# Kernel tuning notes

Hardware: AMD Instinct MI355X
Metric: run time of the kernel (lower is better)

The kernel has to match this reference:

```python
import jax, jax.numpy as jnp
import numpy as np

NUM_CODES = 8192
CODE_DIM = 64
DECAY = 0.99
EPSILON = 1e-05
COMMITMENT_COST = 0.25


def setup_inputs() -> dict:
    key = jax.random.key(0)
    k1, k2, k3 = jax.random.split(key, 3)
    z = jax.random.normal(k1, (32768, CODE_DIM), dtype=jnp.float32)
    emb = jax.random.normal(k2, (NUM_CODES, CODE_DIM), dtype=jnp.float32)
    emb = emb / jnp.linalg.norm(emb, axis=1, keepdims=True)
    return {
        "z": z,
        "embedding": emb,
        "ema_cluster_size": jnp.zeros((NUM_CODES,), dtype=jnp.float32),
        "ema_embedding": emb.copy(),
    }


def reference(z, embedding, ema_cluster_size, ema_embedding):
    z_flat = z.reshape(-1, CODE_DIM)  # [N, D]
    # squared euclidean distances [N, K]
    distances = (
        jnp.sum(z_flat * z_flat, axis=1, keepdims=True)
        - 2.0 * (z_flat @ embedding.T)
        + jnp.sum(embedding * embedding, axis=1)
    )
    indices = jnp.argmin(distances, axis=1)  # [N] int
    z_q = embedding[indices]  # [N, D] gather

    # EMA buffer updates (training path), expressed as pure outputs.
    counts = jax.ops.segment_sum(
        jnp.ones_like(indices, dtype=z_flat.dtype), indices, num_segments=NUM_CODES
    )  # encodings.sum(0)
    dw = jax.ops.segment_sum(z_flat, indices, num_segments=NUM_CODES)  # encodings.T @ z_flat
    new_cluster_size = DECAY * ema_cluster_size + (1.0 - DECAY) * counts
    new_ema_embedding = DECAY * ema_embedding + (1.0 - DECAY) * dw
    n = jnp.sum(new_cluster_size)
    cluster_size = (new_cluster_size + EPSILON) / (n + NUM_CODES * EPSILON) * n
    new_embedding = new_ema_embedding / cluster_size[:, None]

    z_q_full = z_q.reshape(z.shape)
    z_q_st = z + jax.lax.stop_gradient(z_q_full - z)  # straight-through
    vq_loss = COMMITMENT_COST * jnp.mean(
        (jax.lax.stop_gradient(z_q_full) - z) ** 2
    )
    return (z_q_st, indices, vq_loss, new_embedding, new_cluster_size, new_ema_embedding)
```

## Files before the change

### kernel.cpp

```cpp
#include <hip/hip_runtime.h>

typedef _Float16 half8 __attribute__((ext_vector_type(8)));
typedef float f32x4 __attribute__((ext_vector_type(4)));

#define N_PTS   32768
#define DIMS    64
#define K_CODES 8192

#define OUT_ZQ      0
#define OUT_IDX     2097152
#define OUT_LOSS    2129920
#define OUT_NEWEMB  2129921
#define OUT_NCS     2654209
#define OUT_NEWEMA  2662401

#define SC_EHI      0
#define SC_ELO      262144
#define SC_ENSC     524288
#define SC_VAL1     532480
#define SC_IDX1     794624
#define SC_VAL2     1056768
#define SC_FIXLIST  1318912
#define SC_SORTED   1323008
#define SC_OFFSETS  1355776

#define WS_COUNTS   0
#define WS_CURSOR   8192
#define WS_LOSS     16384
#define WS_NSUM     16385
#define WS_FIXCNT   16386
#define WS_ZERO_BYTES (16388u * 4u)
#define WS_NCS      16388
#define WS_ENORM    24580
#define WS_IDX      32772
#define WS_DW       65540

#define MARGIN_SCALED 16.0f

__device__ inline void gld16(const void* g, void* l) {
    __builtin_amdgcn_global_load_lds((const __attribute__((address_space(1))) unsigned*)g,
                                     (__attribute__((address_space(3))) unsigned*)l, 16, 0, 0);
}
__device__ inline void gld4(const void* g, void* l) {
    __builtin_amdgcn_global_load_lds((const __attribute__((address_space(1))) unsigned*)g,
                                     (__attribute__((address_space(3))) unsigned*)l, 4, 0, 0);
}

__global__ __launch_bounds__(256) void esplit_kernel(const float* __restrict__ emb,
                                                     float4* __restrict__ ehi4,
                                                     float4* __restrict__ elo4,
                                                     float* __restrict__ ensc,
                                                     float* __restrict__ enorm) {
    int k = blockIdx.x * 256 + threadIdx.x;
    const float4* e4 = reinterpret_cast<const float4*>(emb + (size_t)k * DIMS);
    float vals[64];
    float sum = 0.0f;
#pragma unroll
    for (int i = 0; i < 16; ++i) {
        float4 v = e4[i];
        vals[i*4+0] = v.x; vals[i*4+1] = v.y; vals[i*4+2] = v.z; vals[i*4+3] = v.w;
        sum = fmaf(v.x, v.x, sum); sum = fmaf(v.y, v.y, sum);
        sum = fmaf(v.z, v.z, sum); sum = fmaf(v.w, v.w, sum);
    }
    enorm[k] = sum;
    ensc[k]  = 65536.0f * sum;
#pragma unroll
    for (int c = 0; c < 8; ++c) {
        union { _Float16 h[8]; float4 v; } uh, ul;
#pragma unroll
        for (int j = 0; j < 8; ++j) {
            float X = 256.0f * vals[c*8+j];
            _Float16 hh = (_Float16)X;
            uh.h[j] = hh;
            ul.h[j] = (_Float16)(X - (float)hh);
        }
        int cc = c ^ (k & 7);
        ehi4[(size_t)k*8 + cc] = uh.v;
        elo4[(size_t)k*8 + cc] = ul.v;
    }
}

__global__ __launch_bounds__(256) void argmin_mfma(const float* __restrict__ z,
                                                   const char* __restrict__ ehi_g,
                                                   const char* __restrict__ elo_g,
                                                   const float* __restrict__ ensc_g,
                                                   float* __restrict__ val1,
                                                   int* __restrict__ idx1,
                                                   float* __restrict__ val2) {
    __shared__ __align__(16) char ebuf[2][2][8192];
    __shared__ float enb[2][64];

    const int tid = threadIdx.x;
    const int w   = tid >> 6;
    const int l   = tid & 63;
    const int l15 = l & 15;
    const int l4  = l >> 4;
    const int bid = blockIdx.x;
    const int rowbase = (bid >> 2) * 128 + w * 32;
    const int c0      = (bid & 3) * 2048;

    half8 ahi[2][2], alo[2][2];
#pragma unroll
    for (int s = 0; s < 2; ++s) {
        const float* zp = z + (size_t)(rowbase + s*16 + l15) * DIMS + l4 * 8;
#pragma unroll
        for (int ks = 0; ks < 2; ++ks) {
            float4 z0 = *reinterpret_cast<const float4*>(zp + ks*32);
            float4 z1 = *reinterpret_cast<const float4*>(zp + ks*32 + 4);
            float xv[8] = {z0.x, z0.y, z0.z, z0.w, z1.x, z1.y, z1.z, z1.w};
            half8 h, lo;
#pragma unroll
            for (int j = 0; j < 8; ++j) {
                float X = -512.0f * xv[j];
                _Float16 hh = (_Float16)X;
                h[j]  = hh;
                lo[j] = (_Float16)(X - (float)hh);
            }
            ahi[s][ks] = h; alo[s][ks] = lo;
        }
    }

    float b1[8], b2[8]; int i1[8];
#pragma unroll
    for (int r = 0; r < 8; ++r) { b1[r] = 3.4e38f; b2[r] = 3.4e38f; i1[r] = 0; }

    int rdoff[2];
#pragma unroll
    for (int ks = 0; ks < 2; ++ks)
        rdoff[ks] = l15 * 128 + (((ks*4 + l4) ^ (l15 & 7)) * 16);

    {
        const size_t gb = (size_t)c0 * 128;
        const char* sh = ehi_g + gb + tid*16;
        const char* sl = elo_g + gb + tid*16;
        char* dh = &ebuf[0][0][0] + w*1024;
        char* dl = &ebuf[0][1][0] + w*1024;
        gld16(sh,        dh);        gld16(sh + 4096, dh + 4096);
        gld16(sl,        dl);        gld16(sl + 4096, dl + 4096);
        if (w == 0) gld4(ensc_g + c0 + l, &enb[0][0]);
    }
    __syncthreads();

    int b = 0;
    for (int ch = 0; ch < 32; ++ch) {
        if (ch < 31) {
            const size_t gb = (size_t)(c0 + (ch+1)*64) * 128;
            const char* sh = ehi_g + gb + tid*16;
            const char* sl = elo_g + gb + tid*16;
            char* dh = &ebuf[b^1][0][0] + w*1024;
            char* dl = &ebuf[b^1][1][0] + w*1024;
            gld16(sh,        dh);        gld16(sh + 4096, dh + 4096);
            gld16(sl,        dl);        gld16(sl + 4096, dl + 4096);
            if (w == 0) gld4(ensc_g + c0 + (ch+1)*64 + l, &enb[b^1][0]);
        }
        const char* bhbase = &ebuf[b][0][0];
        const char* blbase = &ebuf[b][1][0];
#pragma unroll
        for (int t = 0; t < 4; ++t) {
            float en = enb[b][t*16 + l15];
            f32x4 envec = (f32x4){en, en, en, en};
            half8 bh[2], bl[2];
#pragma unroll
            for (int ks = 0; ks < 2; ++ks) {
                bh[ks] = *reinterpret_cast<const half8*>(bhbase + t*2048 + rdoff[ks]);
                bl[ks] = *reinterpret_cast<const half8*>(blbase + t*2048 + rdoff[ks]);
            }
            f32x4 acc[2];
            __builtin_amdgcn_s_setprio(1);
#pragma unroll
            for (int s = 0; s < 2; ++s)
                acc[s] = __builtin_amdgcn_mfma_f32_16x16x32_f16(ahi[s][0], bh[0], envec, 0, 0, 0);
#pragma unroll
            for (int s = 0; s < 2; ++s)
                acc[s] = __builtin_amdgcn_mfma_f32_16x16x32_f16(ahi[s][0], bl[0], acc[s], 0, 0, 0);
#pragma unroll
            for (int s = 0; s < 2; ++s)
                acc[s] = __builtin_amdgcn_mfma_f32_16x16x32_f16(alo[s][0], bh[0], acc[s], 0, 0, 0);
#pragma unroll
            for (int s = 0; s < 2; ++s)
                acc[s] = __builtin_amdgcn_mfma_f32_16x16x32_f16(ahi[s][1], bh[1], acc[s], 0, 0, 0);
#pragma unroll
            for (int s = 0; s < 2; ++s)
                acc[s] = __builtin_amdgcn_mfma_f32_16x16x32_f16(ahi[s][1], bl[1], acc[s], 0, 0, 0);
#pragma unroll
            for (int s = 0; s < 2; ++s)
                acc[s] = __builtin_amdgcn_mfma_f32_16x16x32_f16(alo[s][1], bh[1], acc[s], 0, 0, 0);
            __builtin_amdgcn_s_setprio(0);

            const int code = c0 + ch*64 + t*16 + l15;
#pragma unroll
            for (int s = 0; s < 2; ++s) {
#pragma unroll
                for (int j = 0; j < 4; ++j) {
                    const int r = s*4 + j;
                    float v = acc[s][j];
                    float nb2;
                    asm("v_med3_f32 %0, %1, %2, %3"
                        : "=v"(nb2) : "v"(b1[r]), "v"(b2[r]), "v"(v));
                    b2[r] = nb2;
                    bool c = v < b1[r];
                    b1[r] = c ? v : b1[r];
                    i1[r] = c ? code : i1[r];
                }
            }
        }
        __syncthreads();
        b ^= 1;
    }

#pragma unroll
    for (int m = 1; m < 16; m <<= 1) {
#pragma unroll
        for (int r = 0; r < 8; ++r) {
            float ob1 = __shfl_xor(b1[r], m, 64);
            int   oi1 = __shfl_xor(i1[r], m, 64);
            float ob2 = __shfl_xor(b2[r], m, 64);
            float nb2 = fminf(fminf(b2[r], ob2), fmaxf(b1[r], ob1));
            bool take = (ob1 < b1[r]) || (ob1 == b1[r] && oi1 < i1[r]);
            b1[r] = take ? ob1 : b1[r];
            i1[r] = take ? oi1 : i1[r];
            b2[r] = nb2;
        }
    }
    if (l15 == 0) {
        const int cs = bid & 3;
#pragma unroll
        for (int s = 0; s < 2; ++s)
#pragma unroll
            for (int j = 0; j < 4; ++j) {
                int row = rowbase + s*16 + l4*4 + j;
                int o = cs * N_PTS + row;
                val1[o] = b1[s*4+j];
                idx1[o] = i1[s*4+j];
                val2[o] = b2[s*4+j];
            }
    }
}

__global__ __launch_bounds__(256) void combine_kernel(const float* __restrict__ val1,
                                                      const int* __restrict__ idx1,
                                                      const float* __restrict__ val2,
                                                      int* __restrict__ ws_idx,
                                                      float* __restrict__ out_idxf,
                                                      int* __restrict__ fixcnt,
                                                      int* __restrict__ fixlist,
                                                      float* __restrict__ counts) {
    int row = blockIdx.x * 256 + threadIdx.x;
    float b1 = val1[row]; int i1 = idx1[row]; float b2 = val2[row];
#pragma unroll
    for (int c = 1; c < 4; ++c) {
        float ob1 = val1[c*N_PTS + row];
        int   oi1 = idx1[c*N_PTS + row];
        float ob2 = val2[c*N_PTS + row];
        float nb2 = fminf(fminf(b2, ob2), fmaxf(b1, ob1));
        if (ob1 < b1) { b1 = ob1; i1 = oi1; }
        b2 = nb2;
    }
    ws_idx[row]   = i1;
    out_idxf[row] = (float)i1;
    atomicAdd(&counts[i1], 1.0f);
    if (b2 - b1 < MARGIN_SCALED) {
        int p = atomicAdd(fixcnt, 1);
        if (p < 4096) fixlist[p] = row;
    }
}

__global__ __launch_bounds__(256) void fixup_kernel(const float* __restrict__ z,
                                                    const float* __restrict__ emb,
                                                    const float* __restrict__ enorm,
                                                    const int* __restrict__ fixcnt,
                                                    const int* __restrict__ fixlist,
                                                    int* __restrict__ ws_idx,
                                                    float* __restrict__ out_idxf,
                                                    float* __restrict__ counts) {
    __shared__ float zrow[64];
    __shared__ float rv[256];
    __shared__ int   ri[256];
    int cnt = *fixcnt; if (cnt > 4096) cnt = 4096;
    for (int g = blockIdx.x; g < cnt; g += 64) {
        int row = fixlist[g];
        __syncthreads();
        if (threadIdx.x < 64) zrow[threadIdx.x] = z[(size_t)row * DIMS + threadIdx.x];
        __syncthreads();
        float best = 3.4e38f; int bi = 0;
        for (int k = threadIdx.x; k < K_CODES; k += 256) {
            const float4* e4 = reinterpret_cast<const float4*>(emb + (size_t)k * DIMS);
            float s = 0.0f;
#pragma unroll
            for (int i = 0; i < 16; ++i) {
                float4 ev = e4[i];
                s = fmaf(zrow[i*4+0], ev.x, s);
                s = fmaf(zrow[i*4+1], ev.y, s);
                s = fmaf(zrow[i*4+2], ev.z, s);
                s = fmaf(zrow[i*4+3], ev.w, s);
            }
            float d = fmaf(-2.0f, s, enorm[k]);
            if (d < best) { best = d; bi = k; }
        }
        rv[threadIdx.x] = best; ri[threadIdx.x] = bi;
        __syncthreads();
        for (int off = 128; off > 0; off >>= 1) {
            if (threadIdx.x < off) {
                float ov = rv[threadIdx.x + off]; int oi = ri[threadIdx.x + off];
                if (ov < rv[threadIdx.x] || (ov == rv[threadIdx.x] && oi < ri[threadIdx.x])) {
                    rv[threadIdx.x] = ov; ri[threadIdx.x] = oi;
                }
            }
            __syncthreads();
        }
        if (threadIdx.x == 0) {
            int old = ws_idx[row];
            if (ri[0] != old) {
                atomicAdd(&counts[old], -1.0f);
                atomicAdd(&counts[ri[0]], 1.0f);
                ws_idx[row] = ri[0];
                out_idxf[row] = (float)ri[0];
            }
        }
    }
}

__global__ __launch_bounds__(256) void scan_cs_kernel(const float* __restrict__ ema_cs,
                                                      const float* __restrict__ counts,
                                                      float* __restrict__ ncs_ws,
                                                      float* __restrict__ out_ncs,
                                                      float* __restrict__ nsum,
                                                      int* __restrict__ offsets) {
    __shared__ int excl[256];
    __shared__ int tot[256];
    __shared__ float fpart[256];
    const int t = threadIdx.x;
    const int base = t * 32;
    int loc[32];
    int run = 0;
    float fs = 0.0f;
#pragma unroll
    for (int i = 0; i < 32; ++i) {
        float c = counts[base + i];
        float v = fmaf(0.99f, ema_cs[base + i], 0.01f * c);
        ncs_ws[base + i] = v;
        out_ncs[base + i] = v;
        fs += v;
        loc[i] = run;
        run += (int)c;
    }
    tot[t] = run;
    fpart[t] = fs;
    __syncthreads();
    if (t == 0) {
        int r = 0;
        float f = 0.0f;
        for (int i = 0; i < 256; ++i) { excl[i] = r; r += tot[i]; f += fpart[i]; }
        nsum[0] = f;
    }
    __syncthreads();
    const int off = excl[t];
#pragma unroll
    for (int i = 0; i < 32; ++i) offsets[base + i] = off + loc[i];
}

__global__ __launch_bounds__(256) void place_kernel(const int* __restrict__ idx,
                                                    const int* __restrict__ offsets,
                                                    int* __restrict__ cursor,
                                                    int* __restrict__ sorted) {
    int p = blockIdx.x * 256 + threadIdx.x;
    int k = idx[p];
    int pos = offsets[k] + atomicAdd(&cursor[k], 1);
    sorted[pos] = p;
}

__global__ __launch_bounds__(256) void dw_kernel(const float* __restrict__ z,
                                                 const int* __restrict__ sorted,
                                                 const int* __restrict__ offsets,
                                                 const float* __restrict__ counts,
                                                 float* __restrict__ dw) {
    const int w = threadIdx.x >> 6;
    const int lane = threadIdx.x & 63;
    const int k = blockIdx.x * 4 + w;
    const int start = offsets[k];
    const int cnt = (int)counts[k];
    float s = 0.0f;
    for (int i = 0; i < cnt; ++i) {
        int p = sorted[start + i];
        s += z[(size_t)p * DIMS + lane];
    }
    dw[(size_t)k * DIMS + lane] = s;
}

__global__ __launch_bounds__(256) void scatter_light(const float* __restrict__ z,
                                                     const float* __restrict__ emb,
                                                     const int* __restrict__ idx,
                                                     float* __restrict__ zq_out,
                                                     float* __restrict__ loss_accum) {
    const int tid = threadIdx.x;
    const int p = blockIdx.x * 64 + (tid >> 2);
    const int q = tid & 3;
    const int k = idx[p];

    const float4* zp = reinterpret_cast<const float4*>(z + (size_t)p * DIMS + q * 16);
    const float4* ep = reinterpret_cast<const float4*>(emb + (size_t)k * DIMS + q * 16);
    float4* op = reinterpret_cast<float4*>(zq_out + (size_t)p * DIMS + q * 16);

    float lsum = 0.0f;
#pragma unroll
    for (int i = 0; i < 4; ++i) {
        float4 zv = zp[i];
        float4 ev = ep[i];
        float4 t;
        t.x = ev.x - zv.x; t.y = ev.y - zv.y; t.z = ev.z - zv.z; t.w = ev.w - zv.w;
        lsum = fmaf(t.x, t.x, lsum); lsum = fmaf(t.y, t.y, lsum);
        lsum = fmaf(t.z, t.z, lsum); lsum = fmaf(t.w, t.w, lsum);
        float4 o;
        o.x = zv.x + t.x; o.y = zv.y + t.y; o.z = zv.z + t.z; o.w = zv.w + t.w;
        op[i] = o;
    }
#pragma unroll
    for (int o = 32; o > 0; o >>= 1) lsum += __shfl_down(lsum, o);
    if ((tid & 63) == 0) atomicAdd(loss_accum, lsum);
}

__global__ __launch_bounds__(256) void final_kernel(const float* __restrict__ ema_emb,
                                                    const float* __restrict__ dw,
                                                    const float* __restrict__ ncs,
                                                    const float* __restrict__ n_ptr,
                                                    const float* __restrict__ loss_ptr,
                                                    float* __restrict__ out_newemb,
                                                    float* __restrict__ out_newema,
                                                    float* __restrict__ out_loss) {
    const int i = blockIdx.x * 256 + threadIdx.x;
    const int k = i >> 6;
    const float n = *n_ptr;
    const float cs = (ncs[k] + 1e-5f) / (n + (float)K_CODES * 1e-5f) * n;
    const float ne = fmaf(0.99f, ema_emb[i], 0.01f * dw[i]);
    out_newema[i] = ne;
    out_newemb[i] = ne / cs;
    if (i == 0) out_loss[0] = 0.25f * (loss_ptr[0] / 2097152.0f);
}

extern "C" void kernel_launch(void* const* d_in, const int* in_sizes, int n_in,
                              void* d_out, int out_size, void* d_ws, size_t ws_size,
                              hipStream_t stream) {
    const float* z       = (const float*)d_in[0];
    const float* emb     = (const float*)d_in[1];
    const float* ema_cs  = (const float*)d_in[2];
    const float* ema_emb = (const float*)d_in[3];
    float* out = (float*)d_out;
    float* ws  = (float*)d_ws;

    float* counts  = ws + WS_COUNTS;
    int*   cursor  = (int*)(ws + WS_CURSOR);
    float* loss    = ws + WS_LOSS;
    float* nsum    = ws + WS_NSUM;
    int*   fixcnt  = (int*)(ws + WS_FIXCNT);
    float* ncs     = ws + WS_NCS;
    float* enorm   = ws + WS_ENORM;
    int*   idx     = (int*)(ws + WS_IDX);
    float* dw      = ws + WS_DW;

    float* ehi     = out + SC_EHI;
    float* elo     = out + SC_ELO;
    float* ensc    = out + SC_ENSC;
    float* val1    = out + SC_VAL1;
    int*   idx1    = (int*)(out + SC_IDX1);
    float* val2    = out + SC_VAL2;
    int*   fixlist = (int*)(out + SC_FIXLIST);
    int*   sorted  = (int*)(out + SC_SORTED);
    int*   offsets = (int*)(out + SC_OFFSETS);

    hipMemsetAsync(d_ws, 0, WS_ZERO_BYTES, stream);

    esplit_kernel<<<K_CODES / 256, 256, 0, stream>>>(emb, (float4*)ehi, (float4*)elo, ensc, enorm);

    argmin_mfma<<<1024, 256, 0, stream>>>(z, (const char*)ehi, (const char*)elo, ensc,
                                          val1, idx1, val2);

    combine_kernel<<<N_PTS / 256, 256, 0, stream>>>(val1, idx1, val2, idx, out + OUT_IDX,
                                                    fixcnt, fixlist, counts);

    fixup_kernel<<<64, 256, 0, stream>>>(z, emb, enorm, fixcnt, fixlist, idx, out + OUT_IDX,
                                         counts);

    scan_cs_kernel<<<1, 256, 0, stream>>>(ema_cs, counts, ncs, out + OUT_NCS, nsum, offsets);

    place_kernel<<<N_PTS / 256, 256, 0, stream>>>(idx, offsets, cursor, sorted);

    dw_kernel<<<K_CODES / 4, 256, 0, stream>>>(z, sorted, offsets, counts, dw);

    scatter_light<<<N_PTS / 64, 256, 0, stream>>>(z, emb, idx, out + OUT_ZQ, loss);

    final_kernel<<<(K_CODES * DIMS) / 256, 256, 0, stream>>>(ema_emb, dw, ncs, nsum, loss,
                                                             out + OUT_NEWEMB,
                                                             out + OUT_NEWEMA,
                                                             out + OUT_LOSS);
}
```

Before: 304.6 us.

## Fuse dw into final kernel, shrink fixup margin, widen fixup grid

Result: no change. 301.6 us (-1.0%).

```diff
diff --git a/kernel.cpp b/kernel.cpp
--- a/kernel.cpp
+++ b/kernel.cpp
@@ -21,8 +21,6 @@
 #define SC_IDX1     794624
 #define SC_VAL2     1056768
 #define SC_FIXLIST  1318912
-#define SC_SORTED   1323008
-#define SC_OFFSETS  1355776
 
 #define WS_COUNTS   0
 #define WS_CURSOR   8192
@@ -33,9 +31,10 @@
 #define WS_NCS      16388
 #define WS_ENORM    24580
 #define WS_IDX      32772
-#define WS_DW       65540
-
-#define MARGIN_SCALED 16.0f
+#define WS_SORTED   65540
+#define WS_OFFSETS  98308
+
+#define MARGIN_SCALED 4.0f
 
 __device__ inline void gld16(const void* g, void* l) {
     __builtin_amdgcn_global_load_lds((const __attribute__((address_space(1))) unsigned*)g,
@@ -277,7 +276,7 @@
     __shared__ float rv[256];
     __shared__ int   ri[256];
     int cnt = *fixcnt; if (cnt > 4096) cnt = 4096;
-    for (int g = blockIdx.x; g < cnt; g += 64) {
+    for (int g = blockIdx.x; g < cnt; g += 4096) {
         int row = fixlist[g];
         __syncthreads();
         if (threadIdx.x < 64) zrow[threadIdx.x] = z[(size_t)row * DIMS + threadIdx.x];
@@ -369,24 +368,6 @@
     sorted[pos] = p;
 }
 
-__global__ __launch_bounds__(256) void dw_kernel(const float* __restrict__ z,
-                                                 const int* __restrict__ sorted,
-                                                 const int* __restrict__ offsets,
-                                                 const float* __restrict__ counts,
-                                                 float* __restrict__ dw) {
-    const int w = threadIdx.x >> 6;
-    const int lane = threadIdx.x & 63;
-    const int k = blockIdx.x * 4 + w;
-    const int start = offsets[k];
-    const int cnt = (int)counts[k];
-    float s = 0.0f;
-    for (int i = 0; i < cnt; ++i) {
-        int p = sorted[start + i];
-        s += z[(size_t)p * DIMS + lane];
-    }
-    dw[(size_t)k * DIMS + lane] = s;
-}
-
 __global__ __launch_bounds__(256) void scatter_light(const float* __restrict__ z,
                                                      const float* __restrict__ emb,
                                                      const int* __restrict__ idx,
@@ -419,22 +400,34 @@
     if ((tid & 63) == 0) atomicAdd(loss_accum, lsum);
 }
 
-__global__ __launch_bounds__(256) void final_kernel(const float* __restrict__ ema_emb,
-                                                    const float* __restrict__ dw,
-                                                    const float* __restrict__ ncs,
-                                                    const float* __restrict__ n_ptr,
-                                                    const float* __restrict__ loss_ptr,
-                                                    float* __restrict__ out_newemb,
-                                                    float* __restrict__ out_newema,
-                                                    float* __restrict__ out_loss) {
-    const int i = blockIdx.x * 256 + threadIdx.x;
-    const int k = i >> 6;
+__global__ __launch_bounds__(256) void dw_final(const float* __restrict__ z,
+                                                const int* __restrict__ sorted,
+                                                const int* __restrict__ offsets,
+                                                const float* __restrict__ counts,
+                                                const float* __restrict__ ema_emb,
+                                                const float* __restrict__ ncs,
+                                                const float* __restrict__ n_ptr,
+                                                const float* __restrict__ loss_ptr,
+                                                float* __restrict__ out_newemb,
+                                                float* __restrict__ out_newema,
+                                                float* __restrict__ out_loss) {
+    const int w = threadIdx.x >> 6;
+    const int lane = threadIdx.x & 63;
+    const int k = blockIdx.x * 4 + w;
+    const int start = offsets[k];
+    const int cnt = (int)counts[k];
+    float s = 0.0f;
+    for (int i = 0; i < cnt; ++i) {
+        int p = sorted[start + i];
+        s += z[(size_t)p * DIMS + lane];
+    }
     const float n = *n_ptr;
     const float cs = (ncs[k] + 1e-5f) / (n + (float)K_CODES * 1e-5f) * n;
-    const float ne = fmaf(0.99f, ema_emb[i], 0.01f * dw[i]);
-    out_newema[i] = ne;
-    out_newemb[i] = ne / cs;
-    if (i == 0) out_loss[0] = 0.25f * (loss_ptr[0] / 2097152.0f);
+    const float ne = fmaf(0.99f, ema_emb[(size_t)k * DIMS + lane], 0.01f * s);
+    out_newema[(size_t)k * DIMS + lane] = ne;
+    out_newemb[(size_t)k * DIMS + lane] = ne / cs;
+    if (blockIdx.x == 0 && threadIdx.x == 0)
+        out_loss[0] = 0.25f * (loss_ptr[0] / 2097152.0f);
 }
 
 extern "C" void kernel_launch(void* const* d_in, const int* in_sizes, int n_in,
@@ -455,7 +448,8 @@
     float* ncs     = ws + WS_NCS;
     float* enorm   = ws + WS_ENORM;
     int*   idx     = (int*)(ws + WS_IDX);
-    float* dw      = ws + WS_DW;
+    int*   sorted  = (int*)(ws + WS_SORTED);
+    int*   offsets = (int*)(ws + WS_OFFSETS);
 
     float* ehi     = out + SC_EHI;
     float* elo     = out + SC_ELO;
@@ -464,8 +458,6 @@
     int*   idx1    = (int*)(out + SC_IDX1);
     float* val2    = out + SC_VAL2;
     int*   fixlist = (int*)(out + SC_FIXLIST);
-    int*   sorted  = (int*)(out + SC_SORTED);
-    int*   offsets = (int*)(out + SC_OFFSETS);
 
     hipMemsetAsync(d_ws, 0, WS_ZERO_BYTES, stream);
 
@@ -477,19 +469,17 @@
     combine_kernel<<<N_PTS / 256, 256, 0, stream>>>(val1, idx1, val2, idx, out + OUT_IDX,
                                                     fixcnt, fixlist, counts);
 
-    fixup_kernel<<<64, 256, 0, stream>>>(z, emb, enorm, fixcnt, fixlist, idx, out + OUT_IDX,
-                                         counts);
+    fixup_kernel<<<4096, 256, 0, stream>>>(z, emb, enorm, fixcnt, fixlist, idx, out + OUT_IDX,
+                                           counts);
 
     scan_cs_kernel<<<1, 256, 0, stream>>>(ema_cs, counts, ncs, out + OUT_NCS, nsum, offsets);
 
     place_kernel<<<N_PTS / 256, 256, 0, stream>>>(idx, offsets, cursor, sorted);
 
-    dw_kernel<<<K_CODES / 4, 256, 0, stream>>>(z, sorted, offsets, counts, dw);
-
     scatter_light<<<N_PTS / 64, 256, 0, stream>>>(z, emb, idx, out + OUT_ZQ, loss);
 
-    final_kernel<<<(K_CODES * DIMS) / 256, 256, 0, stream>>>(ema_emb, dw, ncs, nsum, loss,
-                                                             out + OUT_NEWEMB,
-                                                             out + OUT_NEWEMA,
-                                                             out + OUT_LOSS);
-}
+    dw_final<<<K_CODES / 4, 256, 0, stream>>>(z, sorted, offsets, counts, ema_emb, ncs,
+                                              nsum, loss,
+                                              out + OUT_NEWEMB, out + OUT_NEWEMA,
+                                              out + OUT_LOSS);
+}
```
